# Kernel tuning notes

Measured on AMD Instinct MI355X. Metric: run time of the kernel, lower is better.

The kernel has to match this reference:

```python
import jax, jax.numpy as jnp
import numpy as np

D_MODEL = 1024
NUM_HEADS = 16
D_K = D_MODEL // NUM_HEADS
B, S = 4, 2048


def setup_inputs() -> dict:
    key = jax.random.key(0)
    ks = jax.random.split(key, 12)
    scale = 1.0 / np.sqrt(D_MODEL)
    inp = {
        "q": jax.random.normal(ks[0], (B, S, D_MODEL), dtype=jnp.float32),
        "k": jax.random.normal(ks[1], (B, S, D_MODEL), dtype=jnp.float32),
        "v": jax.random.normal(ks[2], (B, S, D_MODEL), dtype=jnp.float32),
        "mask": jnp.ones((B, 1, 1, S), dtype=jnp.int32),
        "Wq": jax.random.normal(ks[3], (D_MODEL, D_MODEL), dtype=jnp.float32) * scale,
        "bq": jnp.zeros((D_MODEL,), dtype=jnp.float32),
        "Wk": jax.random.normal(ks[4], (D_MODEL, D_MODEL), dtype=jnp.float32) * scale,
        "bk": jnp.zeros((D_MODEL,), dtype=jnp.float32),
        "Wv": jax.random.normal(ks[5], (D_MODEL, D_MODEL), dtype=jnp.float32) * scale,
        "bv": jnp.zeros((D_MODEL,), dtype=jnp.float32),
        "Wo": jax.random.normal(ks[6], (D_MODEL, D_MODEL), dtype=jnp.float32) * scale,
        "bo": jnp.zeros((D_MODEL,), dtype=jnp.float32),
    }
    return inp


def reference(q, k, v, mask, Wq, bq, Wk, bk, Wv, bv, Wo, bo):
    b, s, d = q.shape
    # QKV projections (torch Linear: x @ W.T + b; here weights stored as (d,d) used as x @ W + b)
    query = (q @ Wq + bq).reshape(b, s, NUM_HEADS, D_K).transpose(0, 2, 1, 3)  # (b,h,s,dk)
    key_ = (k @ Wk + bk).reshape(b, s, NUM_HEADS, D_K).transpose(0, 2, 1, 3)
    value = (v @ Wv + bv).reshape(b, s, NUM_HEADS, D_K).transpose(0, 2, 1, 3)
    # full score matrix (b,h,s,s), scaled by sqrt(d_k)
    scores = jnp.einsum("bhqd,bhkd->bhqk", query, key_) / jnp.sqrt(jnp.float32(D_K))
    scores = jnp.where(mask == 0, jnp.float32(-jnp.inf), scores)
    attn = jax.nn.softmax(scores, axis=-1)
    # dropout p=0.0 (eval) -> identity
    out = jnp.einsum("bhqk,bhkd->bhqd", attn, value)  # (b,h,s,dk)
    out = out.transpose(0, 2, 1, 3).reshape(b, s, NUM_HEADS * D_K)
    return out @ Wo + bo
```

## Files before the change

### kernel.cpp

```cpp
#include <hip/hip_runtime.h>

typedef __attribute__((ext_vector_type(8)))  short  short8;
typedef __attribute__((ext_vector_type(4)))  short  short4v;
typedef __attribute__((ext_vector_type(4)))  float  f32x4;
typedef __attribute__((ext_vector_type(16))) float  f32x16;
typedef __attribute__((ext_vector_type(8)))  __bf16 bf8_t;
typedef __attribute__((ext_vector_type(4)))  __bf16 bf4_t;
typedef __attribute__((ext_vector_type(2)))  __bf16 bf2_t;
typedef __attribute__((ext_vector_type(4)))  unsigned uint4v;

#define DMODEL 1024
#define SEQ    2048
#define NB     4
#define NH     16
#define MTOT   (NB * SEQ)
#define SCALE_LOG2E 0.18033688011112042f
#define CSTRIDE 544
#define TSPAN   (8 * CSTRIDE)

static __device__ __forceinline__ ushort f2bf(float f) {
  union { float f; unsigned u; } v; v.f = f;
  unsigned r = v.u + 0x7fffu + ((v.u >> 16) & 1u);
  return (ushort)(r >> 16);
}

static __device__ __forceinline__ float fexp2(float x) {
#if __has_builtin(__builtin_amdgcn_exp2f)
  return __builtin_amdgcn_exp2f(x);
#else
  return __expf(x * 0.6931471805599453f);
#endif
}

static __device__ __forceinline__ f32x4 mfma32(short8 a, short8 b, f32x4 c) {
  return __builtin_amdgcn_mfma_f32_16x16x32_bf16(
      __builtin_bit_cast(bf8_t, a), __builtin_bit_cast(bf8_t, b), c, 0, 0, 0);
}

static __device__ __forceinline__ f32x16 mfma3232(short8 a, short8 b, f32x16 c) {
  return __builtin_amdgcn_mfma_f32_32x32x16_bf16(
      __builtin_bit_cast(bf8_t, a), __builtin_bit_cast(bf8_t, b), c, 0, 0, 0);
}

static __device__ __forceinline__ unsigned pk2(float a, float b) {
  bf2_t t; t[0] = (__bf16)a; t[1] = (__bf16)b;
  return __builtin_bit_cast(unsigned, t);
}

static __device__ __forceinline__ void plswap(unsigned& a, unsigned& b) {
  asm volatile("v_permlane32_swap_b32 %0, %1" : "+v"(a), "+v"(b));
}

static __device__ __forceinline__ void gl_lds16(const ushort* g, ushort* l) {
  __builtin_amdgcn_global_load_lds(
      (const __attribute__((address_space(1))) unsigned*)(unsigned long long)g,
      (__attribute__((address_space(3))) unsigned*)(unsigned long long)l,
      16, 0, 0);
}

__global__ __launch_bounds__(256) void cvt3_k(
    const float* __restrict__ q, const float* __restrict__ k,
    const float* __restrict__ v, ushort* __restrict__ qb,
    ushort* __restrict__ kb, ushort* __restrict__ vb) {
  const int z = blockIdx.y;
  const float* src = (z == 0) ? q : (z == 1) ? k : v;
  ushort* dst = (z == 0) ? qb : (z == 1) ? kb : vb;
  const size_t i = ((size_t)blockIdx.x * 256 + threadIdx.x) * 8;
  const float4 a0 = *(const float4*)&src[i];
  const float4 a1 = *(const float4*)&src[i + 4];
  bf8_t c;
  c[0] = (__bf16)a0.x; c[1] = (__bf16)a0.y; c[2] = (__bf16)a0.z; c[3] = (__bf16)a0.w;
  c[4] = (__bf16)a1.x; c[5] = (__bf16)a1.y; c[6] = (__bf16)a1.z; c[7] = (__bf16)a1.w;
  *(short8*)&dst[i] = __builtin_bit_cast(short8, c);
}

__global__ __launch_bounds__(64) void bias_k(const int* __restrict__ mask,
                                             float* __restrict__ biasf,
                                             unsigned* __restrict__ flags) {
  const int t = blockIdx.x * 64 + threadIdx.x;
  const int m = mask[t];
  biasf[t] = m ? 0.f : -1e30f;
  const unsigned long long bal = __ballot(m == 0);
  if (threadIdx.x == 0) flags[blockIdx.x] = (bal != 0ull) ? 1u : 0u;
}

__global__ __launch_bounds__(1024) void wtrans_k(
    const float* __restrict__ Wq, const float* __restrict__ Wk,
    const float* __restrict__ Wv, const float* __restrict__ Wo,
    ushort* __restrict__ Wt) {
  __shared__ float tile[32][33];
  const int z = blockIdx.z;
  const float* W = (z == 0) ? Wq : (z == 1) ? Wk : (z == 2) ? Wv : Wo;
  ushort* out = Wt + (size_t)z * DMODEL * DMODEL;
  const int tx = threadIdx.x, ty = threadIdx.y;
  const int n0 = blockIdx.x * 32, k0 = blockIdx.y * 32;
  tile[ty][tx] = W[(size_t)(k0 + ty) * DMODEL + n0 + tx];
  __syncthreads();
  out[(size_t)(n0 + ty) * DMODEL + k0 + tx] = f2bf(tile[tx][ty]);
}

#define GEMM_BODY(A, Bt)                                                        \
  __shared__ ushort Asm[128 * 64];                                              \
  __shared__ ushort Bsm[128 * 64];                                              \
  const int tid = threadIdx.x;                                                  \
  const int wid = tid >> 6, lane = tid & 63;                                    \
  const int wr = wid >> 1, wc = wid & 1;                                        \
  const int lr = lane & 15, lg = lane >> 4;                                     \
  const int m0 = blockIdx.x * 128, n0 = blockIdx.y * 128;                       \
  const int sr8 = lane >> 3, sg = ((lane & 7) ^ sr8) * 8;                       \
  size_t gA[4], gB[4];                                                          \
  ushort *lA[4], *lB[4];                                                        \
  _Pragma("unroll") for (int j = 0; j < 4; j++) {                               \
    const int ch = wid * 4 + j;                                                 \
    gA[j] = (size_t)(m0 + ch * 8 + sr8) * DMODEL + sg;                          \
    gB[j] = (size_t)(n0 + ch * 8 + sr8) * DMODEL + sg;                          \
    lA[j] = &Asm[ch * 512];                                                     \
    lB[j] = &Bsm[ch * 512];                                                     \
  }                                                                             \
  f32x4 acc[4][4];                                                              \
  _Pragma("unroll") for (int m = 0; m < 4; m++)                                 \
      _Pragma("unroll") for (int n = 0; n < 4; n++)                             \
          acc[m][n] = (f32x4){0.f, 0.f, 0.f, 0.f};                              \
  _Pragma("unroll") for (int j = 0; j < 4; j++) {                               \
    gl_lds16(&A[gA[j]], lA[j]);                                                 \
    gl_lds16(&Bt[gB[j]], lB[j]);                                                \
  }                                                                             \
  const int soff = (lg ^ (lr & 7)) * 8;                                         \
  for (int ks = 0; ks < DMODEL / 64; ++ks) {                                    \
    __syncthreads();                                                            \
    _Pragma("unroll") for (int kk = 0; kk < 2; kk++) {                          \
      const int sx = soff ^ (kk * 32);                                          \
      short8 af[4], bfr[4];                                                     \
      _Pragma("unroll") for (int m = 0; m < 4; m++) af[m] =                     \
          *(const short8*)&Asm[(wr * 64 + m * 16 + lr) * 64 + sx];              \
      _Pragma("unroll") for (int n = 0; n < 4; n++) bfr[n] =                    \
          *(const short8*)&Bsm[(wc * 64 + n * 16 + lr) * 64 + sx];              \
      _Pragma("unroll") for (int m = 0; m < 4; m++)                             \
          _Pragma("unroll") for (int n = 0; n < 4; n++)                         \
              acc[m][n] = mfma32(af[m], bfr[n], acc[m][n]);                     \
    }                                                                           \
    __syncthreads();                                                            \
    if (ks < DMODEL / 64 - 1) {                                                 \
      const size_t ko = (size_t)(ks + 1) * 64;                                  \
      _Pragma("unroll") for (int j = 0; j < 4; j++) {                           \
        gl_lds16(&A[gA[j] + ko], lA[j]);                                        \
        gl_lds16(&Bt[gB[j] + ko], lB[j]);                                       \
      }                                                                         \
    }                                                                           \
  }

__global__ __launch_bounds__(256) void gemmqkv_k(
    const ushort* __restrict__ qb, const ushort* __restrict__ kb,
    const ushort* __restrict__ vb, const ushort* __restrict__ Wt,
    const float* __restrict__ bq, const float* __restrict__ bk,
    const float* __restrict__ bv, ushort* __restrict__ Qp,
    ushort* __restrict__ Kp, ushort* __restrict__ Vb) {
  const int z = blockIdx.z;
  const ushort* A = (z == 0) ? qb : (z == 1) ? kb : vb;
  const ushort* Bt = Wt + (size_t)z * DMODEL * DMODEL;
  const float* bias = (z == 0) ? bq : (z == 1) ? bk : bv;
  GEMM_BODY(A, Bt)
  const float scale = (z == 0) ? SCALE_LOG2E : 1.f;
  float bv4[4];
#pragma unroll
  for (int n = 0; n < 4; n++) bv4[n] = bias[n0 + wc * 64 + n * 16 + lr];
#pragma unroll
  for (int m = 0; m < 4; m++) {
    const int grb = m0 + wr * 64 + m * 16 + lg * 4;
#pragma unroll
    for (int n = 0; n < 4; n++) {
      const int gc = n0 + wc * 64 + n * 16 + lr;
      const int hh = gc >> 6, dk = gc & 63;
      if (z == 2) {
        const int bb = grb >> 11, ss = grb & 2047;
        bf4_t pk;
#pragma unroll
        for (int j = 0; j < 4; j++) pk[j] = (__bf16)(acc[m][n][j] + bv4[n]);
        const size_t addr = (((size_t)bb * NH + hh) * SEQ) * 64 +
                            (size_t)(ss >> 6) * 4096 + dk * 64 +
                            ((ss & 63) ^ ((dk & 7) * 8));
        *(short4v*)&Vb[addr] = __builtin_bit_cast(short4v, pk);
      } else {
#pragma unroll
        for (int j = 0; j < 4; j++) {
          const float val = (acc[m][n][j] + bv4[n]) * scale;
          const int r = grb + j;
          const int b = r >> 11, s = r & 2047;
          if (z == 0) {
            Qp[((((size_t)b * NH + hh) * SEQ) + s) * 64 + dk] =
                __builtin_bit_cast(ushort, (__bf16)val);
          } else {
            const size_t addr = (((size_t)b * NH + hh) * SEQ) * 64 +
                                (size_t)(s >> 6) * 4096 + (s & 63) * 64 +
                                (dk ^ ((s & 7) * 8));
            Kp[addr] = __builtin_bit_cast(ushort, (__bf16)val);
          }
        }
      }
    }
  }
}

__global__ __launch_bounds__(256) void gemmo_k(
    const ushort* __restrict__ Ain, const ushort* __restrict__ Btin,
    const float* __restrict__ bias, float* __restrict__ out) {
  GEMM_BODY(Ain, Btin)
  float bv4[4];
#pragma unroll
  for (int n = 0; n < 4; n++) bv4[n] = bias[n0 + wc * 64 + n * 16 + lr];
#pragma unroll
  for (int m = 0; m < 4; m++) {
    const int grb = m0 + wr * 64 + m * 16 + lg * 4;
#pragma unroll
    for (int n = 0; n < 4; n++) {
      const int gc = n0 + wc * 64 + n * 16 + lr;
#pragma unroll
      for (int j = 0; j < 4; j++)
        out[(size_t)(grb + j) * DMODEL + gc] = acc[m][n][j] + bv4[n];
    }
  }
}

__global__ __launch_bounds__(256) void attn_k(
    const ushort* __restrict__ Qp, const ushort* __restrict__ Kp,
    const ushort* __restrict__ Vt, const float* __restrict__ biasf,
    const unsigned* __restrict__ flags, ushort* __restrict__ ctx) {
  __shared__ ushort smem[4 * TSPAN];
  const int tid = threadIdx.x, w = tid >> 6, lane = tid & 63;
  const int q = lane & 31, hi = lane >> 5;
  const int n = blockIdx.x;
  const int xcd = n & 7, idx = n >> 3;
  const int bh = ((idx >> 4) << 3) | xcd;
  const int qt = idx & 15;
  const int b = bh >> 4, h = bh & 15;
  const int q0w = qt * 128 + w * 32;
  const ushort* Qh = Qp + (size_t)bh * SEQ * 64;
  const ushort* Kh = Kp + (size_t)bh * SEQ * 64;
  const ushort* Vh = Vt + (size_t)bh * SEQ * 64;
  const float* biasb = biasf + b * SEQ;
  const unsigned* flb = flags + b * 32;

  short8 qf[4];
#pragma unroll
  for (int c = 0; c < 4; c++)
    qf[c] = *(const short8*)&Qh[(size_t)(q0w + q) * 64 + c * 16 + hi * 8];

  const int xo = (q & 7) * 8;
  const int rbase = q * 64 + (q >> 3) * 32;
  int off[4];
#pragma unroll
  for (int c = 0; c < 4; c++) off[c] = rbase + ((c * 16 + hi * 8) ^ xo);

  const int sl = lane * 8;
  const int c0 = 2 * w, c1 = 2 * w + 1;

  f32x16 o0, o1;
#pragma unroll
  for (int r = 0; r < 16; r++) { o0[r] = 0.f; o1[r] = 0.f; }
  float l_run = 0.f;

  gl_lds16(&Kh[c0 * 512 + sl], &smem[c0 * CSTRIDE]);
  gl_lds16(&Kh[c1 * 512 + sl], &smem[c1 * CSTRIDE]);
  gl_lds16(&Vh[c0 * 512 + sl], &smem[2 * TSPAN + c0 * CSTRIDE]);
  gl_lds16(&Vh[c1 * 512 + sl], &smem[2 * TSPAN + c1 * CSTRIDE]);
  __syncthreads();

  for (int it = 0; it < 32; ++it) {
    const int cur = it & 1;
    if (it < 31) {
      const size_t tb = (size_t)(it + 1) * 4096;
      ushort* kd = &smem[(cur ^ 1) * TSPAN];
      ushort* vd = &smem[2 * TSPAN + (cur ^ 1) * TSPAN];
      gl_lds16(&Kh[tb + c0 * 512 + sl], &kd[c0 * CSTRIDE]);
      gl_lds16(&Kh[tb + c1 * 512 + sl], &kd[c1 * CSTRIDE]);
      gl_lds16(&Vh[tb + c0 * 512 + sl], &vd[c0 * CSTRIDE]);
      gl_lds16(&Vh[tb + c1 * 512 + sl], &vd[c1 * CSTRIDE]);
    }

    const ushort* kl = &smem[cur * TSPAN];
    const ushort* vl = &smem[2 * TSPAN + cur * TSPAN];

    f32x16 s0, s1;
#pragma unroll
    for (int r = 0; r < 16; r++) { s0[r] = 0.f; s1[r] = 0.f; }
#pragma unroll
    for (int c = 0; c < 4; c++)
      s0 = mfma3232(*(const short8*)&kl[off[c]], qf[c], s0);
#pragma unroll
    for (int c = 0; c < 4; c++)
      s1 = mfma3232(*(const short8*)&kl[off[c] + 2176], qf[c], s1);

    float p[32];
    if (flb[it]) {
      const float* bp = biasb + it * 64;
#pragma unroll
      for (int kt = 0; kt < 2; kt++)
#pragma unroll
        for (int g = 0; g < 4; g++) {
          const f32x4 ba = *(const f32x4*)&bp[kt * 32 + g * 8 + hi * 4];
#pragma unroll
          for (int j = 0; j < 4; j++)
            p[kt * 16 + g * 4 + j] =
                fexp2((kt ? s1[g * 4 + j] : s0[g * 4 + j]) + ba[j]);
        }
    } else {
#pragma unroll
      for (int r = 0; r < 16; r++) {
        p[r] = fexp2(s0[r]);
        p[16 + r] = fexp2(s1[r]);
      }
    }

    float a16[16], a8[8], a4[4];
#pragma unroll
    for (int i = 0; i < 16; i++) a16[i] = p[i] + p[16 + i];
#pragma unroll
    for (int i = 0; i < 8; i++) a8[i] = a16[i] + a16[8 + i];
#pragma unroll
    for (int i = 0; i < 4; i++) a4[i] = a8[i] + a8[4 + i];
    float ps = (a4[0] + a4[1]) + (a4[2] + a4[3]);
    ps += __shfl_xor(ps, 32);
    l_run += ps;

    short8 frag[4];
#pragma unroll
    for (int kb = 0; kb < 4; kb++) {
      unsigned X0 = pk2(p[8 * kb + 0], p[8 * kb + 1]);
      unsigned X1 = pk2(p[8 * kb + 2], p[8 * kb + 3]);
      unsigned Y0 = pk2(p[8 * kb + 4], p[8 * kb + 5]);
      unsigned Y1 = pk2(p[8 * kb + 6], p[8 * kb + 7]);
      plswap(X0, Y0);
      plswap(X1, Y1);
      frag[kb] = __builtin_bit_cast(short8, (uint4v){X0, X1, Y0, Y1});
    }

#pragma unroll
    for (int kb = 0; kb < 4; kb++) {
      o0 = mfma3232(*(const short8*)&vl[off[kb]], frag[kb], o0);
      o1 = mfma3232(*(const short8*)&vl[off[kb] + 2176], frag[kb], o1);
    }

    __syncthreads();
  }

  const float inv = 1.f / l_run;
  ushort* ow = &smem[w * 2176];
#pragma unroll
  for (int r = 0; r < 16; r++) {
    const int dk = (r & 3) + 8 * (r >> 2) + 4 * hi;
    ow[q * 68 + dk] = __builtin_bit_cast(ushort, (__bf16)(o0[r] * inv));
    ow[q * 68 + 32 + dk] = __builtin_bit_cast(ushort, (__bf16)(o1[r] * inv));
  }
  __syncthreads();
  const int sr = lane >> 4, dc = (lane & 15) * 4;
#pragma unroll
  for (int i = 0; i < 8; i++) {
    const int qq = i * 4 + sr;
    const short4v vv = *(const short4v*)&ow[qq * 68 + dc];
    *(short4v*)&ctx[((size_t)b * SEQ + q0w + qq) * DMODEL + h * 64 + dc] = vv;
  }
}

extern "C" void kernel_launch(void* const* d_in, const int* in_sizes, int n_in,
                              void* d_out, int out_size, void* d_ws,
                              size_t ws_size, hipStream_t stream) {
  const float* q    = (const float*)d_in[0];
  const float* k    = (const float*)d_in[1];
  const float* v    = (const float*)d_in[2];
  const int*   mask = (const int*)d_in[3];
  const float* Wq   = (const float*)d_in[4];
  const float* bq   = (const float*)d_in[5];
  const float* Wk   = (const float*)d_in[6];
  const float* bk   = (const float*)d_in[7];
  const float* Wv   = (const float*)d_in[8];
  const float* bv   = (const float*)d_in[9];
  const float* Wo   = (const float*)d_in[10];
  const float* bo   = (const float*)d_in[11];

  char* p = (char*)d_ws;
  ushort* Wt = (ushort*)p; p += (size_t)4 * DMODEL * DMODEL * 2;
  ushort* Qp = (ushort*)p; p += (size_t)MTOT * DMODEL * 2;
  ushort* Kp = (ushort*)p; p += (size_t)MTOT * DMODEL * 2;
  ushort* Vb = (ushort*)p; p += (size_t)MTOT * DMODEL * 2;
  ushort* qb = (ushort*)p; p += (size_t)MTOT * DMODEL * 2;
  ushort* kb = (ushort*)p; p += (size_t)MTOT * DMODEL * 2;
  ushort* vb = (ushort*)p; p += (size_t)MTOT * DMODEL * 2;
  float*  biasf = (float*)p; p += (size_t)NB * SEQ * 4;
  unsigned* flags = (unsigned*)p;
  ushort* ctx = qb;

  wtrans_k<<<dim3(32, 32, 4), dim3(32, 32), 0, stream>>>(Wq, Wk, Wv, Wo, Wt);
  bias_k<<<NB * SEQ / 64, 64, 0, stream>>>(mask, biasf, flags);
  cvt3_k<<<dim3(MTOT * DMODEL / (256 * 8), 3), 256, 0, stream>>>(q, k, v, qb,
                                                                 kb, vb);

  gemmqkv_k<<<dim3(MTOT / 128, DMODEL / 128, 3), 256, 0, stream>>>(
      qb, kb, vb, Wt, bq, bk, bv, Qp, Kp, Vb);

  attn_k<<<1024, 256, 0, stream>>>(Qp, Kp, Vb, biasf, flags, ctx);

  gemmo_k<<<dim3(MTOT / 128, DMODEL / 128), 256, 0, stream>>>(
      ctx, Wt + (size_t)3 * DMODEL * DMODEL, bo, (float*)d_out);
}
```

Before: 209.3 us.

## Fold mask bias into convert kernel and compute softmax row sums via MFMA

Removes the separate bias/flag kernel launch by having the first 32 blocks of the q conversion kernel build the mask bias and per-64-key flags. In the attention loop, the per-row sum of probabilities is now taken by an extra MFMA against a vector of bf16 ones, replacing the scalar add tree and cross-lane shuffle. The QK score MFMAs are interleaved and start from a zero accumulator. This adds MFMA work and sums the bf16-rounded probabilities rather than the fp32 ones, which slightly changes the normalisation.

```diff
diff --git a/kernel.cpp b/kernel.cpp
--- a/kernel.cpp
+++ b/kernel.cpp
@@ -61,8 +61,18 @@
 __global__ __launch_bounds__(256) void cvt3_k(
     const float* __restrict__ q, const float* __restrict__ k,
     const float* __restrict__ v, ushort* __restrict__ qb,
-    ushort* __restrict__ kb, ushort* __restrict__ vb) {
+    ushort* __restrict__ kb, ushort* __restrict__ vb,
+    const int* __restrict__ mask, float* __restrict__ biasf,
+    unsigned* __restrict__ flags) {
   const int z = blockIdx.y;
+  if (z == 0 && blockIdx.x < 32) {
+    const int t = blockIdx.x * 256 + threadIdx.x;
+    const int m = mask[t];
+    biasf[t] = m ? 0.f : -1e30f;
+    const unsigned long long bal = __ballot(m == 0);
+    if ((threadIdx.x & 63) == 0)
+      flags[blockIdx.x * 4 + (threadIdx.x >> 6)] = (bal != 0ull) ? 1u : 0u;
+  }
   const float* src = (z == 0) ? q : (z == 1) ? k : v;
   ushort* dst = (z == 0) ? qb : (z == 1) ? kb : vb;
   const size_t i = ((size_t)blockIdx.x * 256 + threadIdx.x) * 8;
@@ -72,16 +82,6 @@
   c[0] = (__bf16)a0.x; c[1] = (__bf16)a0.y; c[2] = (__bf16)a0.z; c[3] = (__bf16)a0.w;
   c[4] = (__bf16)a1.x; c[5] = (__bf16)a1.y; c[6] = (__bf16)a1.z; c[7] = (__bf16)a1.w;
   *(short8*)&dst[i] = __builtin_bit_cast(short8, c);
-}
-
-__global__ __launch_bounds__(64) void bias_k(const int* __restrict__ mask,
-                                             float* __restrict__ biasf,
-                                             unsigned* __restrict__ flags) {
-  const int t = blockIdx.x * 64 + threadIdx.x;
-  const int m = mask[t];
-  biasf[t] = m ? 0.f : -1e30f;
-  const unsigned long long bal = __ballot(m == 0);
-  if (threadIdx.x == 0) flags[blockIdx.x] = (bal != 0ull) ? 1u : 0u;
 }
 
 __global__ __launch_bounds__(1024) void wtrans_k(
@@ -254,10 +254,13 @@
   const int sl = lane * 8;
   const int c0 = 2 * w, c1 = 2 * w + 1;
 
-  f32x16 o0, o1;
-#pragma unroll
-  for (int r = 0; r < 16; r++) { o0[r] = 0.f; o1[r] = 0.f; }
-  float l_run = 0.f;
+  f32x16 o0, o1, lacc, zf;
+#pragma unroll
+  for (int r = 0; r < 16; r++) {
+    o0[r] = 0.f; o1[r] = 0.f; lacc[r] = 0.f; zf[r] = 0.f;
+  }
+  const short ONE = (short)0x3F80;
+  const short8 ones8 = {ONE, ONE, ONE, ONE, ONE, ONE, ONE, ONE};
 
   gl_lds16(&Kh[c0 * 512 + sl], &smem[c0 * CSTRIDE]);
   gl_lds16(&Kh[c1 * 512 + sl], &smem[c1 * CSTRIDE]);
@@ -280,15 +283,13 @@
     const ushort* kl = &smem[cur * TSPAN];
     const ushort* vl = &smem[2 * TSPAN + cur * TSPAN];
 
-    f32x16 s0, s1;
-#pragma unroll
-    for (int r = 0; r < 16; r++) { s0[r] = 0.f; s1[r] = 0.f; }
-#pragma unroll
-    for (int c = 0; c < 4; c++)
+    f32x16 s0 = mfma3232(*(const short8*)&kl[off[0]], qf[0], zf);
+    f32x16 s1 = mfma3232(*(const short8*)&kl[off[0] + 2176], qf[0], zf);
+#pragma unroll
+    for (int c = 1; c < 4; c++) {
       s0 = mfma3232(*(const short8*)&kl[off[c]], qf[c], s0);
-#pragma unroll
-    for (int c = 0; c < 4; c++)
       s1 = mfma3232(*(const short8*)&kl[off[c] + 2176], qf[c], s1);
+    }
 
     float p[32];
     if (flb[it]) {
@@ -310,17 +311,6 @@
         p[16 + r] = fexp2(s1[r]);
       }
     }
-
-    float a16[16], a8[8], a4[4];
-#pragma unroll
-    for (int i = 0; i < 16; i++) a16[i] = p[i] + p[16 + i];
-#pragma unroll
-    for (int i = 0; i < 8; i++) a8[i] = a16[i] + a16[8 + i];
-#pragma unroll
-    for (int i = 0; i < 4; i++) a4[i] = a8[i] + a8[4 + i];
-    float ps = (a4[0] + a4[1]) + (a4[2] + a4[3]);
-    ps += __shfl_xor(ps, 32);
-    l_run += ps;
 
     short8 frag[4];
 #pragma unroll
@@ -338,12 +328,13 @@
     for (int kb = 0; kb < 4; kb++) {
       o0 = mfma3232(*(const short8*)&vl[off[kb]], frag[kb], o0);
       o1 = mfma3232(*(const short8*)&vl[off[kb] + 2176], frag[kb], o1);
+      lacc = mfma3232(ones8, frag[kb], lacc);
     }
 
     __syncthreads();
   }
 
-  const float inv = 1.f / l_run;
+  const float inv = 1.f / lacc[0];
   ushort* ow = &smem[w * 2176];
 #pragma unroll
   for (int r = 0; r < 16; r++) {
@@ -390,9 +381,8 @@
   ushort* ctx = qb;
 
   wtrans_k<<<dim3(32, 32, 4), dim3(32, 32), 0, stream>>>(Wq, Wk, Wv, Wo, Wt);
-  bias_k<<<NB * SEQ / 64, 64, 0, stream>>>(mask, biasf, flags);
-  cvt3_k<<<dim3(MTOT * DMODEL / (256 * 8), 3), 256, 0, stream>>>(q, k, v, qb,
-                                                                 kb, vb);
+  cvt3_k<<<dim3(MTOT * DMODEL / (256 * 8), 3), 256, 0, stream>>>(
+      q, k, v, qb, kb, vb, mask, biasf, flags);
 
   gemmqkv_k<<<dim3(MTOT / 128, DMODEL / 128, 3), 256, 0, stream>>>(
       qb, kb, vb, Wt, bq, bk, bv, Qp, Kp, Vb);
```

New measurement: 210.3 us. No clear change (+0.5%).

## Fuse mask-bias kernel into cvt3 and swap GEMM operands for vectorized Q/K stores

Applied to the files above, without the earlier changes.

Folds the mask-to-bias and flag computation into the input-conversion kernel, which removes one kernel launch. For the Q and K projections the GEMM is computed transposed (W^T times X^T), so each lane's accumulator runs along the head dimension. That lets the epilogue write packed 4-element bf16 vectors instead of scattered scalar stores. The V path is unchanged. The grid mapping changes, and the swizzled K store still depends on dk0 staying 4-aligned.

```diff
diff --git a/kernel.cpp b/kernel.cpp
--- a/kernel.cpp
+++ b/kernel.cpp
@@ -14,6 +14,7 @@
 #define NB     4
 #define NH     16
 #define MTOT   (NB * SEQ)
+#define DM2    ((size_t)DMODEL * DMODEL)
 #define SCALE_LOG2E 0.18033688011112042f
 #define CSTRIDE 544
 #define TSPAN   (8 * CSTRIDE)
@@ -61,8 +62,18 @@
 __global__ __launch_bounds__(256) void cvt3_k(
     const float* __restrict__ q, const float* __restrict__ k,
     const float* __restrict__ v, ushort* __restrict__ qb,
-    ushort* __restrict__ kb, ushort* __restrict__ vb) {
+    ushort* __restrict__ kb, ushort* __restrict__ vb,
+    const int* __restrict__ mask, float* __restrict__ biasf,
+    unsigned* __restrict__ flags) {
   const int z = blockIdx.y;
+  if (z == 0 && blockIdx.x < 32) {
+    const int t = blockIdx.x * 256 + threadIdx.x;
+    const int m = mask[t];
+    biasf[t] = m ? 0.f : -1e30f;
+    const unsigned long long bal = __ballot(m == 0);
+    if ((threadIdx.x & 63) == 0)
+      flags[blockIdx.x * 4 + (threadIdx.x >> 6)] = (bal != 0ull) ? 1u : 0u;
+  }
   const float* src = (z == 0) ? q : (z == 1) ? k : v;
   ushort* dst = (z == 0) ? qb : (z == 1) ? kb : vb;
   const size_t i = ((size_t)blockIdx.x * 256 + threadIdx.x) * 8;
@@ -74,16 +85,6 @@
   *(short8*)&dst[i] = __builtin_bit_cast(short8, c);
 }
 
-__global__ __launch_bounds__(64) void bias_k(const int* __restrict__ mask,
-                                             float* __restrict__ biasf,
-                                             unsigned* __restrict__ flags) {
-  const int t = blockIdx.x * 64 + threadIdx.x;
-  const int m = mask[t];
-  biasf[t] = m ? 0.f : -1e30f;
-  const unsigned long long bal = __ballot(m == 0);
-  if (threadIdx.x == 0) flags[blockIdx.x] = (bal != 0ull) ? 1u : 0u;
-}
-
 __global__ __launch_bounds__(1024) void wtrans_k(
     const float* __restrict__ Wq, const float* __restrict__ Wk,
     const float* __restrict__ Wv, const float* __restrict__ Wo,
@@ -91,7 +92,7 @@
   __shared__ float tile[32][33];
   const int z = blockIdx.z;
   const float* W = (z == 0) ? Wq : (z == 1) ? Wk : (z == 2) ? Wv : Wo;
-  ushort* out = Wt + (size_t)z * DMODEL * DMODEL;
+  ushort* out = Wt + (size_t)z * DM2;
   const int tx = threadIdx.x, ty = threadIdx.y;
   const int n0 = blockIdx.x * 32, k0 = blockIdx.y * 32;
   tile[ty][tx] = W[(size_t)(k0 + ty) * DMODEL + n0 + tx];
@@ -99,14 +100,14 @@
   out[(size_t)(n0 + ty) * DMODEL + k0 + tx] = f2bf(tile[tx][ty]);
 }
 
-#define GEMM_BODY(A, Bt)                                                        \
+#define GEMM_BODY(A, Bt, M0v, N0v)                                              \
   __shared__ ushort Asm[128 * 64];                                              \
   __shared__ ushort Bsm[128 * 64];                                              \
   const int tid = threadIdx.x;                                                  \
   const int wid = tid >> 6, lane = tid & 63;                                    \
   const int wr = wid >> 1, wc = wid & 1;                                        \
   const int lr = lane & 15, lg = lane >> 4;                                     \
-  const int m0 = blockIdx.x * 128, n0 = blockIdx.y * 128;                       \
+  const int m0 = (M0v), n0 = (N0v);                                             \
   const int sr8 = lane >> 3, sg = ((lane & 7) ^ sr8) * 8;                       \
   size_t gA[4], gB[4];                                                          \
   ushort *lA[4], *lB[4];                                                        \
@@ -156,22 +157,24 @@
     const float* __restrict__ bv, ushort* __restrict__ Qp,
     ushort* __restrict__ Kp, ushort* __restrict__ Vb) {
   const int z = blockIdx.z;
-  const ushort* A = (z == 0) ? qb : (z == 1) ? kb : vb;
-  const ushort* Bt = Wt + (size_t)z * DMODEL * DMODEL;
-  const float* bias = (z == 0) ? bq : (z == 1) ? bk : bv;
-  GEMM_BODY(A, Bt)
-  const float scale = (z == 0) ? SCALE_LOG2E : 1.f;
-  float bv4[4];
-#pragma unroll
-  for (int n = 0; n < 4; n++) bv4[n] = bias[n0 + wc * 64 + n * 16 + lr];
-#pragma unroll
-  for (int m = 0; m < 4; m++) {
-    const int grb = m0 + wr * 64 + m * 16 + lg * 4;
-#pragma unroll
-    for (int n = 0; n < 4; n++) {
-      const int gc = n0 + wc * 64 + n * 16 + lr;
-      const int hh = gc >> 6, dk = gc & 63;
-      if (z == 2) {
+  const int bx = blockIdx.x, by = blockIdx.y;
+  const ushort* A  = (z == 0) ? Wt : (z == 1) ? (Wt + DM2) : vb;
+  const ushort* Bm = (z == 0) ? qb : (z == 1) ? kb : (Wt + 2 * DM2);
+  const int M0 = (z == 2) ? bx * 128 : by * 128;
+  const int N0 = (z == 2) ? by * 128 : bx * 128;
+  GEMM_BODY(A, Bm, M0, N0)
+
+  if (z == 2) {
+    float bv4[4];
+#pragma unroll
+    for (int n = 0; n < 4; n++) bv4[n] = bv[n0 + wc * 64 + n * 16 + lr];
+#pragma unroll
+    for (int m = 0; m < 4; m++) {
+      const int grb = m0 + wr * 64 + m * 16 + lg * 4;
+#pragma unroll
+      for (int n = 0; n < 4; n++) {
+        const int gc = n0 + wc * 64 + n * 16 + lr;
+        const int hh = gc >> 6, dk = gc & 63;
         const int bb = grb >> 11, ss = grb & 2047;
         bf4_t pk;
 #pragma unroll
@@ -180,22 +183,33 @@
                             (size_t)(ss >> 6) * 4096 + dk * 64 +
                             ((ss & 63) ^ ((dk & 7) * 8));
         *(short4v*)&Vb[addr] = __builtin_bit_cast(short4v, pk);
-      } else {
-#pragma unroll
-        for (int j = 0; j < 4; j++) {
-          const float val = (acc[m][n][j] + bv4[n]) * scale;
-          const int r = grb + j;
-          const int b = r >> 11, s = r & 2047;
-          if (z == 0) {
-            Qp[((((size_t)b * NH + hh) * SEQ) + s) * 64 + dk] =
-                __builtin_bit_cast(ushort, (__bf16)val);
-          } else {
-            const size_t addr = (((size_t)b * NH + hh) * SEQ) * 64 +
-                                (size_t)(s >> 6) * 4096 + (s & 63) * 64 +
-                                (dk ^ ((s & 7) * 8));
-            Kp[addr] = __builtin_bit_cast(ushort, (__bf16)val);
-          }
+      }
+    }
+  } else {
+    const float* bias = (z == 0) ? bq : bk;
+    ushort* out = (z == 0) ? Qp : Kp;
+    const float scale = (z == 0) ? SCALE_LOG2E : 1.f;
+#pragma unroll
+    for (int m = 0; m < 4; m++) {
+      const int f0 = m0 + wr * 64 + m * 16 + lg * 4;
+      const f32x4 b4 = *(const f32x4*)&bias[f0];
+      const int hh = f0 >> 6, dk0 = f0 & 63;
+#pragma unroll
+      for (int n = 0; n < 4; n++) {
+        const int t = n0 + wc * 64 + n * 16 + lr;
+        const int b = t >> 11, s = t & 2047;
+        bf4_t pk;
+#pragma unroll
+        for (int j = 0; j < 4; j++)
+          pk[j] = (__bf16)((acc[m][n][j] + b4[j]) * scale);
+        size_t addr;
+        if (z == 0) {
+          addr = (((size_t)b * NH + hh) * SEQ + s) * 64 + dk0;
+        } else {
+          addr = (((size_t)b * NH + hh) * SEQ) * 64 + (size_t)(s >> 6) * 4096 +
+                 (s & 63) * 64 + (dk0 ^ ((s & 7) * 8));
         }
+        *(short4v*)&out[addr] = __builtin_bit_cast(short4v, pk);
       }
     }
   }
@@ -204,7 +218,7 @@
 __global__ __launch_bounds__(256) void gemmo_k(
     const ushort* __restrict__ Ain, const ushort* __restrict__ Btin,
     const float* __restrict__ bias, float* __restrict__ out) {
-  GEMM_BODY(Ain, Btin)
+  GEMM_BODY(Ain, Btin, blockIdx.x * 128, blockIdx.y * 128)
   float bv4[4];
 #pragma unroll
   for (int n = 0; n < 4; n++) bv4[n] = bias[n0 + wc * 64 + n * 16 + lr];
@@ -378,7 +392,7 @@
   const float* bo   = (const float*)d_in[11];
 
   char* p = (char*)d_ws;
-  ushort* Wt = (ushort*)p; p += (size_t)4 * DMODEL * DMODEL * 2;
+  ushort* Wt = (ushort*)p; p += (size_t)4 * DM2 * 2;
   ushort* Qp = (ushort*)p; p += (size_t)MTOT * DMODEL * 2;
   ushort* Kp = (ushort*)p; p += (size_t)MTOT * DMODEL * 2;
   ushort* Vb = (ushort*)p; p += (size_t)MTOT * DMODEL * 2;
@@ -390,9 +404,8 @@
   ushort* ctx = qb;
 
   wtrans_k<<<dim3(32, 32, 4), dim3(32, 32), 0, stream>>>(Wq, Wk, Wv, Wo, Wt);
-  bias_k<<<NB * SEQ / 64, 64, 0, stream>>>(mask, biasf, flags);
-  cvt3_k<<<dim3(MTOT * DMODEL / (256 * 8), 3), 256, 0, stream>>>(q, k, v, qb,
-                                                                 kb, vb);
+  cvt3_k<<<dim3(MTOT * DMODEL / (256 * 8), 3), 256, 0, stream>>>(
+      q, k, v, qb, kb, vb, mask, biasf, flags);
 
   gemmqkv_k<<<dim3(MTOT / 128, DMODEL / 128, 3), 256, 0, stream>>>(
       qb, kb, vb, Wt, bq, bk, bv, Qp, Kp, Vb);
@@ -400,5 +413,5 @@
   attn_k<<<1024, 256, 0, stream>>>(Qp, Kp, Vb, biasf, flags, ctx);
 
   gemmo_k<<<dim3(MTOT / 128, DMODEL / 128), 256, 0, stream>>>(
-      ctx, Wt + (size_t)3 * DMODEL * DMODEL, bo, (float*)d_out);
-}
+      ctx, Wt + (size_t)3 * DM2, bo, (float*)d_out);
+}
```

New measurement: 208.8 us. No clear change (-0.2%).
